# Kernel tuning notes

Hardware: AMD Instinct MI355X
Metric: run time of the kernel (lower is better)

## Reference

```python
import jax, jax.numpy as jnp
import numpy as np

NUM_HEADS = 12

def setup_inputs() -> dict:
    key = jax.random.key(0)
    k1, k2, k3, k4 = jax.random.split(key, 4)
    B, N, C = 64, 197, 768
    x = jax.random.normal(k1, (B, N, C), dtype=jnp.float32)
    w_qkv = jax.random.normal(k2, (3 * C, C), dtype=jnp.float32) * (C ** -0.5)
    w_proj = jax.random.normal(k3, (C, C), dtype=jnp.float32) * (C ** -0.5)
    b_proj = jax.random.normal(k4, (C,), dtype=jnp.float32) * 0.01
    return {"x": x, "w_qkv": w_qkv, "w_proj": w_proj, "b_proj": b_proj}

def reference(x, w_qkv, w_proj, b_proj):
    B, N, C = x.shape
    H = NUM_HEADS
    hd = C // H
    scale = hd ** -0.5
    # qkv linear (no bias): [B,N,3C] -> [3,B,H,N,hd]
    qkv = jnp.einsum('bnc,dc->bnd', x, w_qkv).reshape(B, N, 3, H, hd)
    qkv = jnp.transpose(qkv, (2, 0, 3, 1, 4))
    q, k, v = qkv[0], qkv[1], qkv[2]
    # full attention matrix [B,H,N,N] (materialized, matching the original)
    attn = jax.nn.softmax(jnp.einsum('bhnd,bhmd->bhnm', q, k) * scale, axis=-1)
    # CLS-token attention stats: mean over heads of attn row 0 (patch tokens) -> [B, N-1]
    global_attn = jnp.mean(attn[:, :, 0, 1:], axis=1)
    out = jnp.einsum('bhnm,bhmd->bhnd', attn, v)          # [B,H,N,hd]
    out = jnp.transpose(out, (0, 2, 1, 3)).reshape(B, N, C)
    out = jnp.einsum('bnc,dc->bnd', out, w_proj) + b_proj
    return out, global_attn
```

## Files before the change

kernel.cpp:

```cpp
#include <hip/hip_runtime.h>
#include <math.h>

#define B_   64
#define N_   197
#define C_   768
#define H_   12
#define HD_  64
#define BH_  (B_ * H_)
#define M_   (B_ * N_)

typedef _Float16 half8 __attribute__((ext_vector_type(8)));
typedef float    f32x4 __attribute__((ext_vector_type(4)));

#define XH_OFF   0u
#define WQH_OFF  19365888u
#define WPH_OFF  22904832u
#define QH_OFF   24084480u
#define KH_OFF   43450368u
#define VH_OFF   62816256u
#define OH_OFF   82182144u
#define P0_OFF   101548032u
#define WS_BYTES 102150144u

__device__ __forceinline__ half8 h8zero() {
    half8 z;
    #pragma unroll
    for (int i = 0; i < 8; ++i) z[i] = (_Float16)0;
    return z;
}

__device__ __forceinline__ void async16(const _Float16* g, _Float16* l) {
    __builtin_amdgcn_global_load_lds(
        (const __attribute__((address_space(1))) void*)g,
        (__attribute__((address_space(3))) void*)l,
        16, 0, 0);
}

__device__ __forceinline__ int xcd_swz(int i, int nwg) {
    const int q = nwg >> 3, r = nwg & 7;
    const int xcd = i & 7, j = i >> 3;
    return (xcd < r ? xcd * (q + 1) : r * (q + 1) + (xcd - r) * q) + j;
}

__global__ void k_ws_too_small(float* out, float ws_bytes) { out[0] = -ws_bytes; }

__global__ __launch_bounds__(256) void k_cvt_all(const float* __restrict__ x,
                                                 const float* __restrict__ wq,
                                                 const float* __restrict__ wp,
                                                 _Float16* __restrict__ Xh,
                                                 _Float16* __restrict__ Wqh,
                                                 _Float16* __restrict__ Wph) {
    int i = blockIdx.x * blockDim.x + threadIdx.x;
    const float* src;
    _Float16*    dst;
    if (i < 1210368)      { src = x;  dst = Xh; }
    else if (i < 1431552) { src = wq; dst = Wqh; i -= 1210368; }
    else                  { src = wp; dst = Wph; i -= 1431552; }
    float4 f0 = *(const float4*)(src + (size_t)i * 8);
    float4 f1 = *(const float4*)(src + (size_t)i * 8 + 4);
    half8 h;
    h[0]=(_Float16)f0.x; h[1]=(_Float16)f0.y; h[2]=(_Float16)f0.z; h[3]=(_Float16)f0.w;
    h[4]=(_Float16)f1.x; h[5]=(_Float16)f1.y; h[6]=(_Float16)f1.z; h[7]=(_Float16)f1.w;
    *(half8*)(dst + (size_t)i * 8) = h;
}

__device__ __forceinline__ void mfma_nt_core_256(const _Float16* __restrict__ A,
                                                 const _Float16* __restrict__ B,
                                                 int M, int K, int m0, int n0,
                                                 _Float16* As, _Float16* Bs,
                                                 f32x4 (&acc)[8][4]) {
    const int tid  = threadIdx.x;
    const int lane = tid & 63;
    const int w    = tid >> 6;
    const int wm   = w >> 2, wn = w & 3;
    const int ln   = lane & 15, kq = lane >> 4;

    const int srow = tid >> 3;
    const int kcs  = (((tid & 7) ^ (srow & 7)) << 3);
    int ra00 = m0 +       srow; if (ra00 >= M) ra00 = 0;
    int ra01 = m0 +  64 + srow; if (ra01 >= M) ra01 = 0;
    int ra10 = m0 + 128 + srow; if (ra10 >= M) ra10 = 0;
    int ra11 = m0 + 192 + srow; if (ra11 >= M) ra11 = 0;
    const _Float16* A00 = A + (size_t)ra00 * K + kcs;
    const _Float16* A01 = A + (size_t)ra01 * K + kcs;
    const _Float16* A10 = A + (size_t)ra10 * K + kcs;
    const _Float16* A11 = A + (size_t)ra11 * K + kcs;
    const _Float16* B00 = B + (size_t)(n0 +       srow) * K + kcs;
    const _Float16* B01 = B + (size_t)(n0 +  64 + srow) * K + kcs;
    const _Float16* B10 = B + (size_t)(n0 + 128 + srow) * K + kcs;
    const _Float16* B11 = B + (size_t)(n0 + 192 + srow) * K + kcs;
    const int dOff = w << 9;

    const int kx    = (ln & 7) << 3;
    const int aBase = wm * 8192 + ln * 64;
    const int bBase = (wn >> 1) * 8192 + (wn & 1) * 4096 + ln * 64;

    half8 af[4][2], bf[4][2];

    async16(A00, As + dOff);          async16(A01, As + 4096 + dOff);
    async16(A10, As + 8192 + dOff);   async16(A11, As + 12288 + dOff);
    async16(B00, Bs + dOff);          async16(B01, Bs + 4096 + dOff);
    async16(B10, Bs + 8192 + dOff);   async16(B11, Bs + 12288 + dOff);

    const int NT = K >> 6;
    #pragma unroll 1
    for (int t = 0; t < NT; ++t) {
        const int cur  = (t & 1) << 14;
        const int nb   = 16384 - cur;
        const int koff = (t + 1) << 6;
        const bool pre = (t + 1 < NT);
        const _Float16* Ac = As + cur;
        const _Float16* Bc = Bs + cur;

        if (pre) {
            async16(A00 + koff, As + nb + dOff);
            async16(A01 + koff, As + nb + 4096 + dOff);
            async16(A10 + koff, As + nb + 8192 + dOff);
            async16(A11 + koff, As + nb + 12288 + dOff);
            asm volatile("s_waitcnt vmcnt(4)" ::: "memory");
        } else {
            asm volatile("s_waitcnt vmcnt(0)" ::: "memory");
        }
        __builtin_amdgcn_s_barrier();
        __builtin_amdgcn_sched_barrier(0);
        #pragma unroll
        for (int m4 = 0; m4 < 4; ++m4)
            #pragma unroll
            for (int kk = 0; kk < 2; ++kk)
                af[m4][kk] = *(const half8*)&Ac[aBase + m4 * 1024 + ((kk * 32 + kq * 8) ^ kx)];
        #pragma unroll
        for (int n2 = 0; n2 < 2; ++n2)
            #pragma unroll
            for (int kk = 0; kk < 2; ++kk)
                bf[n2][kk] = *(const half8*)&Bc[bBase + n2 * 1024 + ((kk * 32 + kq * 8) ^ kx)];
        __builtin_amdgcn_s_setprio(1);
        #pragma unroll
        for (int m4 = 0; m4 < 4; ++m4)
            #pragma unroll
            for (int n2 = 0; n2 < 2; ++n2)
                #pragma unroll
                for (int kk = 0; kk < 2; ++kk)
                    acc[m4][n2] = __builtin_amdgcn_mfma_f32_16x16x32_f16(af[m4][kk], bf[n2][kk], acc[m4][n2], 0, 0, 0);
        __builtin_amdgcn_s_setprio(0);
        __builtin_amdgcn_sched_barrier(0);
        __builtin_amdgcn_s_barrier();

        if (pre) {
            async16(B00 + koff, Bs + nb + dOff);
            async16(B01 + koff, Bs + nb + 4096 + dOff);
        }
        #pragma unroll
        for (int n2 = 0; n2 < 2; ++n2)
            #pragma unroll
            for (int kk = 0; kk < 2; ++kk)
                bf[2 + n2][kk] = *(const half8*)&Bc[bBase + (2 + n2) * 1024 + ((kk * 32 + kq * 8) ^ kx)];
        __builtin_amdgcn_s_setprio(1);
        #pragma unroll
        for (int m4 = 0; m4 < 4; ++m4)
            #pragma unroll
            for (int n2 = 0; n2 < 2; ++n2)
                #pragma unroll
                for (int kk = 0; kk < 2; ++kk)
                    acc[m4][2 + n2] = __builtin_amdgcn_mfma_f32_16x16x32_f16(af[m4][kk], bf[2 + n2][kk], acc[m4][2 + n2], 0, 0, 0);
        __builtin_amdgcn_s_setprio(0);
        __builtin_amdgcn_sched_barrier(0);
        __builtin_amdgcn_s_barrier();

        if (pre) {
            async16(B10 + koff, Bs + nb + 8192 + dOff);
            async16(B11 + koff, Bs + nb + 12288 + dOff);
        }
        #pragma unroll
        for (int m4 = 0; m4 < 4; ++m4)
            #pragma unroll
            for (int kk = 0; kk < 2; ++kk)
                af[m4][kk] = *(const half8*)&Ac[aBase + (4 + m4) * 1024 + ((kk * 32 + kq * 8) ^ kx)];
        __builtin_amdgcn_s_setprio(1);
        #pragma unroll
        for (int m4 = 0; m4 < 4; ++m4)
            #pragma unroll
            for (int n2 = 0; n2 < 2; ++n2)
                #pragma unroll
                for (int kk = 0; kk < 2; ++kk)
                    acc[4 + m4][n2] = __builtin_amdgcn_mfma_f32_16x16x32_f16(af[m4][kk], bf[n2][kk], acc[4 + m4][n2], 0, 0, 0);
        __builtin_amdgcn_s_setprio(0);
        __builtin_amdgcn_sched_barrier(0);
        __builtin_amdgcn_s_barrier();

        __builtin_amdgcn_s_setprio(1);
        #pragma unroll
        for (int m4 = 0; m4 < 4; ++m4)
            #pragma unroll
            for (int n2 = 0; n2 < 2; ++n2)
                #pragma unroll
                for (int kk = 0; kk < 2; ++kk)
                    acc[4 + m4][2 + n2] = __builtin_amdgcn_mfma_f32_16x16x32_f16(af[m4][kk], bf[2 + n2][kk], acc[4 + m4][2 + n2], 0, 0, 0);
        __builtin_amdgcn_s_setprio(0);
        asm volatile("s_waitcnt lgkmcnt(0)" ::: "memory");
        __builtin_amdgcn_sched_barrier(0);
        __builtin_amdgcn_s_barrier();
    }
}

__global__ __launch_bounds__(512, 2) void k_qkv_mfma(const _Float16* __restrict__ Xh,
                                                     const _Float16* __restrict__ Wq,
                                                     _Float16* __restrict__ Qh,
                                                     _Float16* __restrict__ Kh,
                                                     _Float16* __restrict__ Vh) {
    __shared__ _Float16 As[32768];
    __shared__ _Float16 Bs[32768];
    const int work = xcd_swz(blockIdx.x, 50 * 9);
    const int m0 = (work / 9) << 8;
    const int n0 = (work % 9) << 8;
    f32x4 acc[8][4] = {};
    mfma_nt_core_256(Xh, Wq, M_, C_, m0, n0, As, Bs, acc);

    const int lane = threadIdx.x & 63;
    const int w    = threadIdx.x >> 6;
    const int wm = w >> 2, wn = w & 3;
    const int ln = lane & 15, kq = lane >> 4;

    _Float16* basep[4];
    float     scl[4];
    #pragma unroll
    for (int ni = 0; ni < 4; ++ni) {
        const int d  = n0 + wn * 64 + ni * 16 + ln;
        const int t3 = d / C_;
        const int rr = d - t3 * C_;
        const int h  = rr >> 6;
        const int e  = rr & 63;
        _Float16* tp = (t3 == 0) ? Qh : (t3 == 1) ? Kh : Vh;
        basep[ni] = tp + (size_t)h * N_ * HD_ + e;
        scl[ni]   = (t3 == 0) ? 0.125f : 1.f;
    }
    #pragma unroll
    for (int mi = 0; mi < 8; ++mi) {
        #pragma unroll
        for (int i = 0; i < 4; ++i) {
            const int m = m0 + wm * 128 + mi * 16 + kq * 4 + i;
            if (m >= M_) continue;
            const int b = m / N_;
            const int n = m - b * N_;
            const size_t rowoff = ((size_t)b * H_ * N_ + n) * HD_;
            #pragma unroll
            for (int ni = 0; ni < 4; ++ni)
                basep[ni][rowoff] = (_Float16)(acc[mi][ni][i] * scl[ni]);
        }
    }
}

__global__ __launch_bounds__(512, 2) void k_proj_mfma(const _Float16* __restrict__ Oh,
                                                      const _Float16* __restrict__ Wp,
                                                      const float* __restrict__ bias,
                                                      float* __restrict__ out) {
    __shared__ _Float16 As[32768];
    __shared__ _Float16 Bs[32768];
    const int work = xcd_swz(blockIdx.x, 50 * 3);
    const int m0 = (work / 3) << 8;
    const int n0 = (work % 3) << 8;
    f32x4 acc[8][4] = {};
    mfma_nt_core_256(Oh, Wp, M_, C_, m0, n0, As, Bs, acc);

    const int lane = threadIdx.x & 63;
    const int w    = threadIdx.x >> 6;
    const int wm = w >> 2, wn = w & 3;
    const int ln = lane & 15, kq = lane >> 4;
    float bv[4];
    #pragma unroll
    for (int ni = 0; ni < 4; ++ni) bv[ni] = bias[n0 + wn * 64 + ni * 16 + ln];
    #pragma unroll
    for (int mi = 0; mi < 8; ++mi) {
        #pragma unroll
        for (int i = 0; i < 4; ++i) {
            const int m = m0 + wm * 128 + mi * 16 + kq * 4 + i;
            if (m >= M_) continue;
            #pragma unroll
            for (int ni = 0; ni < 4; ++ni)
                out[(size_t)m * C_ + n0 + wn * 64 + ni * 16 + ln] = acc[mi][ni][i] + bv[ni];
        }
    }
}

__global__ __launch_bounds__(256) void k_attn(const _Float16* __restrict__ Qh,
                                              const _Float16* __restrict__ Kh,
                                              const _Float16* __restrict__ Vh,
                                              _Float16* __restrict__ Oh,
                                              float* __restrict__ P0) {
    __shared__ _Float16 lds[29824];
    _Float16* Ks = lds;
    _Float16* Pl = lds;
    _Float16* Vt = lds + 14976;

    const int work = xcd_swz(blockIdx.y * 4 + blockIdx.x, 4 * BH_);
    const int bh = work >> 2, rt = work & 3;
    const int b = bh / H_, h = bh - b * H_;
    const int tid = threadIdx.x, wave = tid >> 6, lane = tid & 63;
    const int ln = lane & 15, kq = lane >> 4;
    const size_t kvb = (size_t)bh * N_ * HD_;

    for (int idx = tid; idx < 208 * 8; idx += 256) {
        const int key = idx >> 3, c = (idx & 7) << 3;
        half8 v = (key < N_) ? *(const half8*)(Kh + kvb + (size_t)key * HD_ + c) : h8zero();
        *(half8*)&Ks[key * 72 + c] = v;
    }
    for (int idx = tid; idx < 197 * 8; idx += 256) {
        const int key = idx >> 3, c = (idx & 7) << 3;
        half8 v = *(const half8*)(Vh + kvb + (size_t)key * HD_ + c);
        #pragma unroll
        for (int j = 0; j < 8; ++j) Vt[(c + j) * 232 + key] = v[j];
    }
    for (int idx = tid; idx < 64 * 27; idx += 256) {
        const int d = idx / 27, k = 197 + (idx - d * 27);
        Vt[d * 232 + k] = (_Float16)0;
    }
    const int qrow = rt * 64 + wave * 16 + ln;
    const _Float16* Qp = Qh + kvb + (size_t)((qrow < N_) ? qrow : 0) * HD_ + kq * 8;
    half8 qf0 = *(const half8*)Qp;
    half8 qf1 = *(const half8*)(Qp + 32);
    __syncthreads();

    f32x4 acc[13] = {};
    __builtin_amdgcn_s_setprio(1);
    #pragma unroll
    for (int c = 0; c < 13; ++c) {
        const _Float16* kp = &Ks[(c * 16 + ln) * 72 + kq * 8];
        half8 kf0 = *(const half8*)kp;
        half8 kf1 = *(const half8*)(kp + 32);
        acc[c] = __builtin_amdgcn_mfma_f32_16x16x32_f16(qf0, kf0, acc[c], 0, 0, 0);
        acc[c] = __builtin_amdgcn_mfma_f32_16x16x32_f16(qf1, kf1, acc[c], 0, 0, 0);
    }
    __builtin_amdgcn_s_setprio(0);
    float inv4[4];
    #pragma unroll
    for (int r = 0; r < 4; ++r) {
        float m = -1e30f;
        #pragma unroll
        for (int c = 0; c < 13; ++c) {
            float x = ((c * 16 + ln) < N_) ? acc[c][r] : -1e30f;
            acc[c][r] = x;
            m = fmaxf(m, x);
        }
        m = fmaxf(m, __shfl_xor(m, 1)); m = fmaxf(m, __shfl_xor(m, 2));
        m = fmaxf(m, __shfl_xor(m, 4)); m = fmaxf(m, __shfl_xor(m, 8));
        float s = 0.f;
        #pragma unroll
        for (int c = 0; c < 13; ++c) { float e = __expf(acc[c][r] - m); acc[c][r] = e; s += e; }
        s += __shfl_xor(s, 1); s += __shfl_xor(s, 2);
        s += __shfl_xor(s, 4); s += __shfl_xor(s, 8);
        inv4[r] = 1.f / s;
    }
    __syncthreads();

    _Float16* Pw = Pl + wave * 16 * 232;
    #pragma unroll
    for (int c = 0; c < 13; ++c) {
        const int col = c * 16 + ln;
        #pragma unroll
        for (int r = 0; r < 4; ++r)
            Pw[(kq * 4 + r) * 232 + col] = (_Float16)(acc[c][r] * inv4[r]);
    }
    #pragma unroll
    for (int r = 0; r < 4; ++r) Pw[(kq * 4 + r) * 232 + 208 + ln] = (_Float16)0;

    if (rt == 0 && wave == 0 && kq == 0) {
        #pragma unroll
        for (int c = 0; c < 13; ++c) {
            const int col = c * 16 + ln;
            if (col >= 1 && col < N_) P0[(size_t)bh * 196 + col - 1] = acc[c][0] * inv4[0];
        }
    }
    __syncthreads();

    f32x4 o4[4] = {};
    __builtin_amdgcn_s_setprio(1);
    for (int t = 0; t < 7; ++t) {
        half8 pf = *(const half8*)&Pw[ln * 232 + kq * 8 + 32 * t];
        #pragma unroll
        for (int n = 0; n < 4; ++n) {
            half8 vf = *(const half8*)&Vt[(n * 16 + ln) * 232 + kq * 8 + 32 * t];
            o4[n] = __builtin_amdgcn_mfma_f32_16x16x32_f16(pf, vf, o4[n], 0, 0, 0);
        }
    }
    __builtin_amdgcn_s_setprio(0);
    const int g0 = rt * 64 + wave * 16 + kq * 4;
    #pragma unroll
    for (int r = 0; r < 4; ++r) {
        const int g = g0 + r;
        if (g >= N_) continue;
        _Float16* op = Oh + ((size_t)b * N_ + g) * C_ + h * HD_;
        #pragma unroll
        for (int n = 0; n < 4; ++n) op[n * 16 + ln] = (_Float16)o4[n][r];
    }
}

__global__ void k_gattn(const float* __restrict__ P0, float* __restrict__ out2) {
    const int idx = blockIdx.x * blockDim.x + threadIdx.x;
    const int b = idx / (N_ - 1), m = idx - b * (N_ - 1);
    float s = 0.f;
    #pragma unroll
    for (int h = 0; h < H_; ++h) s += P0[((size_t)(b * H_ + h)) * 196 + m];
    out2[idx] = s * (1.f / H_);
}

extern "C" void kernel_launch(void* const* d_in, const int* in_sizes, int n_in,
                              void* d_out, int out_size, void* d_ws, size_t ws_size,
                              hipStream_t stream) {
    const float* x      = (const float*)d_in[0];
    const float* w_qkv  = (const float*)d_in[1];
    const float* w_proj = (const float*)d_in[2];
    const float* b_proj = (const float*)d_in[3];
    float* out = (float*)d_out;
    char* ws   = (char*)d_ws;

    if (ws_size < (size_t)WS_BYTES) {
        k_ws_too_small<<<1, 1, 0, stream>>>(out, (float)ws_size);
        return;
    }

    _Float16* Xh  = (_Float16*)(ws + XH_OFF);
    _Float16* Wqh = (_Float16*)(ws + WQH_OFF);
    _Float16* Wph = (_Float16*)(ws + WPH_OFF);
    _Float16* Qh  = (_Float16*)(ws + QH_OFF);
    _Float16* Kh  = (_Float16*)(ws + KH_OFF);
    _Float16* Vh  = (_Float16*)(ws + VH_OFF);
    _Float16* Oh  = (_Float16*)(ws + OH_OFF);
    float*    P0  = (float*)   (ws + P0_OFF);

    k_cvt_all<<<5880, 256, 0, stream>>>(x, w_qkv, w_proj, Xh, Wqh, Wph);

    k_qkv_mfma <<<dim3(450), 512, 0, stream>>>(Xh, Wqh, Qh, Kh, Vh);
    k_attn     <<<dim3(4, BH_), 256, 0, stream>>>(Qh, Kh, Vh, Oh, P0);
    k_gattn    <<<dim3(49),     256, 0, stream>>>(P0, out + (size_t)M_ * C_);
    k_proj_mfma<<<dim3(150), 512, 0, stream>>>(Oh, Wph, b_proj, out);
}
```

Before: 249.7 us.

## Load K/V once per head in attention and retile projection GEMM to 128x128

```diff
diff --git a/kernel.cpp b/kernel.cpp
--- a/kernel.cpp
+++ b/kernel.cpp
@@ -202,6 +202,60 @@
     }
 }
 
+__device__ __forceinline__ void mfma_nt_core_h(const _Float16* __restrict__ A,
+                                               const _Float16* __restrict__ B,
+                                               int M, int K, int m0, int n0,
+                                               _Float16* As, _Float16* Bs,
+                                               f32x4 (&acc)[4][4]) {
+    const int tid  = threadIdx.x;
+    const int wave = tid >> 6, lane = tid & 63;
+    const int wr   = (wave >> 1) << 6;
+    const int wc   = (wave & 1) << 6;
+    const int ln   = lane & 15, kq = lane >> 4;
+
+    const int row0 = tid >> 2;
+    const int ch0  = (tid & 3) << 3;
+    int ar0 = m0 + row0;        if (ar0 >= M) ar0 = 0;
+    int ar1 = m0 + 64 + row0;   if (ar1 >= M) ar1 = 0;
+    const _Float16* A0 = A + (size_t)ar0 * K + ch0;
+    const _Float16* A1 = A + (size_t)ar1 * K + ch0;
+    const _Float16* B0 = B + (size_t)(n0 + row0) * K + ch0;
+    const _Float16* B1 = B + (size_t)(n0 + 64 + row0) * K + ch0;
+    _Float16* AsD = As + (wave << 9);
+    _Float16* BsD = Bs + (wave << 9);
+
+    async16(A0, AsD);        async16(A1, AsD + 2048);
+    async16(B0, BsD);        async16(B1, BsD + 2048);
+    __syncthreads();
+
+    int cur = 0;
+    for (int k0 = 0; k0 < K; k0 += 32) {
+        const int nxt = cur ^ 1;
+        if (k0 + 32 < K) {
+            const int nb = nxt << 12;
+            async16(A0 + k0 + 32, AsD + nb);
+            async16(A1 + k0 + 32, AsD + nb + 2048);
+            async16(B0 + k0 + 32, BsD + nb);
+            async16(B1 + k0 + 32, BsD + nb + 2048);
+        }
+        const _Float16* Ac = As + (cur << 12);
+        const _Float16* Bc = Bs + (cur << 12);
+        half8 af[4], bf[4];
+        #pragma unroll
+        for (int t = 0; t < 4; ++t) {
+            af[t] = *(const half8*)&Ac[(wr + t * 16 + ln) * 32 + kq * 8];
+            bf[t] = *(const half8*)&Bc[(wc + t * 16 + ln) * 32 + kq * 8];
+        }
+        #pragma unroll
+        for (int i = 0; i < 4; ++i)
+            #pragma unroll
+            for (int j = 0; j < 4; ++j)
+                acc[i][j] = __builtin_amdgcn_mfma_f32_16x16x32_f16(af[i], bf[j], acc[i][j], 0, 0, 0);
+        __syncthreads();
+        cur = nxt;
+    }
+}
+
 __global__ __launch_bounds__(512, 2) void k_qkv_mfma(const _Float16* __restrict__ Xh,
                                                      const _Float16* __restrict__ Wq,
                                                      _Float16* __restrict__ Qh,
@@ -249,34 +303,34 @@
     }
 }
 
-__global__ __launch_bounds__(512, 2) void k_proj_mfma(const _Float16* __restrict__ Oh,
-                                                      const _Float16* __restrict__ Wp,
-                                                      const float* __restrict__ bias,
-                                                      float* __restrict__ out) {
-    __shared__ _Float16 As[32768];
-    __shared__ _Float16 Bs[32768];
-    const int work = xcd_swz(blockIdx.x, 50 * 3);
-    const int m0 = (work / 3) << 8;
-    const int n0 = (work % 3) << 8;
-    f32x4 acc[8][4] = {};
-    mfma_nt_core_256(Oh, Wp, M_, C_, m0, n0, As, Bs, acc);
+__global__ __launch_bounds__(256) void k_proj_mfma(const _Float16* __restrict__ Oh,
+                                                   const _Float16* __restrict__ Wp,
+                                                   const float* __restrict__ bias,
+                                                   float* __restrict__ out) {
+    __shared__ _Float16 As[2 * 4096];
+    __shared__ _Float16 Bs[2 * 4096];
+    const int work = xcd_swz(blockIdx.y * 6 + blockIdx.x, 6 * 99);
+    const int m0 = (work / 6) << 7;
+    const int n0 = (work % 6) << 7;
+    f32x4 acc[4][4] = {};
+    mfma_nt_core_h(Oh, Wp, M_, C_, m0, n0, As, Bs, acc);
 
     const int lane = threadIdx.x & 63;
-    const int w    = threadIdx.x >> 6;
-    const int wm = w >> 2, wn = w & 3;
+    const int wave = threadIdx.x >> 6;
+    const int wr = (wave >> 1) << 6, wc = (wave & 1) << 6;
     const int ln = lane & 15, kq = lane >> 4;
     float bv[4];
     #pragma unroll
-    for (int ni = 0; ni < 4; ++ni) bv[ni] = bias[n0 + wn * 64 + ni * 16 + ln];
+    for (int nt = 0; nt < 4; ++nt) bv[nt] = bias[n0 + wc + nt * 16 + ln];
     #pragma unroll
-    for (int mi = 0; mi < 8; ++mi) {
+    for (int mt = 0; mt < 4; ++mt) {
         #pragma unroll
         for (int i = 0; i < 4; ++i) {
-            const int m = m0 + wm * 128 + mi * 16 + kq * 4 + i;
+            const int m = m0 + wr + mt * 16 + kq * 4 + i;
             if (m >= M_) continue;
             #pragma unroll
-            for (int ni = 0; ni < 4; ++ni)
-                out[(size_t)m * C_ + n0 + wn * 64 + ni * 16 + ln] = acc[mi][ni][i] + bv[ni];
+            for (int nt = 0; nt < 4; ++nt)
+                out[(size_t)m * C_ + n0 + wc + nt * 16 + ln] = acc[mt][nt][i] + bv[nt];
         }
     }
 }
@@ -286,110 +340,127 @@
                                               const _Float16* __restrict__ Vh,
                                               _Float16* __restrict__ Oh,
                                               float* __restrict__ P0) {
-    __shared__ _Float16 lds[29824];
+    __shared__ _Float16 lds[39936];
     _Float16* Ks = lds;
-    _Float16* Pl = lds;
-    _Float16* Vt = lds + 14976;
-
-    const int work = xcd_swz(blockIdx.y * 4 + blockIdx.x, 4 * BH_);
-    const int bh = work >> 2, rt = work & 3;
+    _Float16* Vt = lds + 13312;
+    _Float16* Pl = lds + 26624;
+
+    const int bh = blockIdx.x;
     const int b = bh / H_, h = bh - b * H_;
     const int tid = threadIdx.x, wave = tid >> 6, lane = tid & 63;
     const int ln = lane & 15, kq = lane >> 4;
     const size_t kvb = (size_t)bh * N_ * HD_;
 
     for (int idx = tid; idx < 208 * 8; idx += 256) {
-        const int key = idx >> 3, c = (idx & 7) << 3;
-        half8 v = (key < N_) ? *(const half8*)(Kh + kvb + (size_t)key * HD_ + c) : h8zero();
-        *(half8*)&Ks[key * 72 + c] = v;
+        const int key = idx >> 3, c8 = idx & 7;
+        half8 v = (key < N_) ? *(const half8*)(Kh + kvb + (size_t)key * HD_ + c8 * 8) : h8zero();
+        *(half8*)&Ks[key * 64 + ((c8 ^ (key & 7)) << 3)] = v;
     }
     for (int idx = tid; idx < 197 * 8; idx += 256) {
         const int key = idx >> 3, c = (idx & 7) << 3;
         half8 v = *(const half8*)(Vh + kvb + (size_t)key * HD_ + c);
         #pragma unroll
-        for (int j = 0; j < 8; ++j) Vt[(c + j) * 232 + key] = v[j];
-    }
-    for (int idx = tid; idx < 64 * 27; idx += 256) {
-        const int d = idx / 27, k = 197 + (idx - d * 27);
-        Vt[d * 232 + k] = (_Float16)0;
-    }
-    const int qrow = rt * 64 + wave * 16 + ln;
-    const _Float16* Qp = Qh + kvb + (size_t)((qrow < N_) ? qrow : 0) * HD_ + kq * 8;
-    half8 qf0 = *(const half8*)Qp;
-    half8 qf1 = *(const half8*)(Qp + 32);
+        for (int j = 0; j < 8; ++j) Vt[(c + j) * 208 + key] = v[j];
+    }
+    for (int idx = tid; idx < 64 * 11; idx += 256) {
+        const int d = idx / 11, k = 197 + (idx - d * 11);
+        Vt[d * 208 + k] = (_Float16)0;
+    }
     __syncthreads();
 
-    f32x4 acc[13] = {};
-    __builtin_amdgcn_s_setprio(1);
-    #pragma unroll
-    for (int c = 0; c < 13; ++c) {
-        const _Float16* kp = &Ks[(c * 16 + ln) * 72 + kq * 8];
-        half8 kf0 = *(const half8*)kp;
-        half8 kf1 = *(const half8*)(kp + 32);
-        acc[c] = __builtin_amdgcn_mfma_f32_16x16x32_f16(qf0, kf0, acc[c], 0, 0, 0);
-        acc[c] = __builtin_amdgcn_mfma_f32_16x16x32_f16(qf1, kf1, acc[c], 0, 0, 0);
-    }
-    __builtin_amdgcn_s_setprio(0);
-    float inv4[4];
-    #pragma unroll
-    for (int r = 0; r < 4; ++r) {
-        float m = -1e30f;
+    _Float16* Pw = Pl + wave * 16 * 208;
+    const int swz = ln & 7;
+
+    for (int rt = 0; rt < 4; ++rt) {
+        if (rt * 64 + wave * 16 >= N_) continue;
+
+        const int qrow = rt * 64 + wave * 16 + ln;
+        const _Float16* Qp = Qh + kvb + (size_t)((qrow < N_) ? qrow : 0) * HD_ + kq * 8;
+        half8 qf0 = *(const half8*)Qp;
+        half8 qf1 = *(const half8*)(Qp + 32);
+
+        f32x4 acc[13] = {};
+        __builtin_amdgcn_s_setprio(1);
         #pragma unroll
         for (int c = 0; c < 13; ++c) {
-            float x = ((c * 16 + ln) < N_) ? acc[c][r] : -1e30f;
-            acc[c][r] = x;
-            m = fmaxf(m, x);
-        }
-        m = fmaxf(m, __shfl_xor(m, 1)); m = fmaxf(m, __shfl_xor(m, 2));
-        m = fmaxf(m, __shfl_xor(m, 4)); m = fmaxf(m, __shfl_xor(m, 8));
-        float s = 0.f;
-        #pragma unroll
-        for (int c = 0; c < 13; ++c) { float e = __expf(acc[c][r] - m); acc[c][r] = e; s += e; }
-        s += __shfl_xor(s, 1); s += __shfl_xor(s, 2);
-        s += __shfl_xor(s, 4); s += __shfl_xor(s, 8);
-        inv4[r] = 1.f / s;
-    }
-    __syncthreads();
-
-    _Float16* Pw = Pl + wave * 16 * 232;
-    #pragma unroll
-    for (int c = 0; c < 13; ++c) {
-        const int col = c * 16 + ln;
-        #pragma unroll
-        for (int r = 0; r < 4; ++r)
-            Pw[(kq * 4 + r) * 232 + col] = (_Float16)(acc[c][r] * inv4[r]);
-    }
-    #pragma unroll
-    for (int r = 0; r < 4; ++r) Pw[(kq * 4 + r) * 232 + 208 + ln] = (_Float16)0;
-
-    if (rt == 0 && wave == 0 && kq == 0) {
+            const _Float16* kp = &Ks[(c * 16 + ln) * 64];
+            half8 kf0 = *(const half8*)(kp + ((kq ^ swz) << 3));
+            half8 kf1 = *(const half8*)(kp + (((4 + kq) ^ swz) << 3));
+            acc[c] = __builtin_amdgcn_mfma_f32_16x16x32_f16(qf0, kf0, acc[c], 0, 0, 0);
+            acc[c] = __builtin_amdgcn_mfma_f32_16x16x32_f16(qf1, kf1, acc[c], 0, 0, 0);
+        }
+        __builtin_amdgcn_s_setprio(0);
+
+        float inv4[4];
+        #pragma unroll
+        for (int r = 0; r < 4; ++r) {
+            float m = -1e30f;
+            #pragma unroll
+            for (int c = 0; c < 13; ++c) {
+                float x = ((c * 16 + ln) < N_) ? acc[c][r] : -1e30f;
+                acc[c][r] = x;
+                m = fmaxf(m, x);
+            }
+            m = fmaxf(m, __shfl_xor(m, 1)); m = fmaxf(m, __shfl_xor(m, 2));
+            m = fmaxf(m, __shfl_xor(m, 4)); m = fmaxf(m, __shfl_xor(m, 8));
+            float s = 0.f;
+            #pragma unroll
+            for (int c = 0; c < 13; ++c) { float e = __expf(acc[c][r] - m); acc[c][r] = e; s += e; }
+            s += __shfl_xor(s, 1); s += __shfl_xor(s, 2);
+            s += __shfl_xor(s, 4); s += __shfl_xor(s, 8);
+            inv4[r] = 1.f / s;
+        }
+
         #pragma unroll
         for (int c = 0; c < 13; ++c) {
             const int col = c * 16 + ln;
-            if (col >= 1 && col < N_) P0[(size_t)bh * 196 + col - 1] = acc[c][0] * inv4[0];
-        }
-    }
-    __syncthreads();
-
-    f32x4 o4[4] = {};
-    __builtin_amdgcn_s_setprio(1);
-    for (int t = 0; t < 7; ++t) {
-        half8 pf = *(const half8*)&Pw[ln * 232 + kq * 8 + 32 * t];
-        #pragma unroll
-        for (int n = 0; n < 4; ++n) {
-            half8 vf = *(const half8*)&Vt[(n * 16 + ln) * 232 + kq * 8 + 32 * t];
-            o4[n] = __builtin_amdgcn_mfma_f32_16x16x32_f16(pf, vf, o4[n], 0, 0, 0);
-        }
-    }
-    __builtin_amdgcn_s_setprio(0);
-    const int g0 = rt * 64 + wave * 16 + kq * 4;
-    #pragma unroll
-    for (int r = 0; r < 4; ++r) {
-        const int g = g0 + r;
-        if (g >= N_) continue;
-        _Float16* op = Oh + ((size_t)b * N_ + g) * C_ + h * HD_;
-        #pragma unroll
-        for (int n = 0; n < 4; ++n) op[n * 16 + ln] = (_Float16)o4[n][r];
+            #pragma unroll
+            for (int r = 0; r < 4; ++r)
+                Pw[(kq * 4 + r) * 208 + col] = (_Float16)(acc[c][r] * inv4[r]);
+        }
+
+        if (rt == 0 && wave == 0 && kq == 0) {
+            #pragma unroll
+            for (int c = 0; c < 13; ++c) {
+                const int col = c * 16 + ln;
+                if (col >= 1 && col < N_) P0[(size_t)bh * 196 + col - 1] = acc[c][0] * inv4[0];
+            }
+        }
+        asm volatile("s_waitcnt lgkmcnt(0)" ::: "memory");
+        __builtin_amdgcn_sched_barrier(0);
+
+        f32x4 o4[4] = {};
+        __builtin_amdgcn_s_setprio(1);
+        #pragma unroll
+        for (int t = 0; t < 6; ++t) {
+            half8 pf = *(const half8*)&Pw[ln * 208 + kq * 8 + 32 * t];
+            #pragma unroll
+            for (int n = 0; n < 4; ++n) {
+                half8 vf = *(const half8*)&Vt[(n * 16 + ln) * 208 + kq * 8 + 32 * t];
+                o4[n] = __builtin_amdgcn_mfma_f32_16x16x32_f16(pf, vf, o4[n], 0, 0, 0);
+            }
+        }
+        {
+            const int off6 = (kq < 2) ? (192 + kq * 8) : 0;
+            half8 pf = *(const half8*)&Pw[ln * 208 + off6];
+            if (kq >= 2) pf = h8zero();
+            #pragma unroll
+            for (int n = 0; n < 4; ++n) {
+                half8 vf = *(const half8*)&Vt[(n * 16 + ln) * 208 + off6];
+                o4[n] = __builtin_amdgcn_mfma_f32_16x16x32_f16(pf, vf, o4[n], 0, 0, 0);
+            }
+        }
+        __builtin_amdgcn_s_setprio(0);
+
+        const int g0 = rt * 64 + wave * 16 + kq * 4;
+        #pragma unroll
+        for (int r = 0; r < 4; ++r) {
+            const int g = g0 + r;
+            if (g >= N_) continue;
+            _Float16* op = Oh + ((size_t)b * N_ + g) * C_ + h * HD_;
+            #pragma unroll
+            for (int n = 0; n < 4; ++n) op[n * 16 + ln] = (_Float16)o4[n][r];
+        }
     }
 }
 
@@ -428,8 +499,8 @@
 
     k_cvt_all<<<5880, 256, 0, stream>>>(x, w_qkv, w_proj, Xh, Wqh, Wph);
 
-    k_qkv_mfma <<<dim3(450), 512, 0, stream>>>(Xh, Wqh, Qh, Kh, Vh);
-    k_attn     <<<dim3(4, BH_), 256, 0, stream>>>(Qh, Kh, Vh, Oh, P0);
-    k_gattn    <<<dim3(49),     256, 0, stream>>>(P0, out + (size_t)M_ * C_);
-    k_proj_mfma<<<dim3(150), 512, 0, stream>>>(Oh, Wph, b_proj, out);
-}
+    k_qkv_mfma <<<dim3(450),   512, 0, stream>>>(Xh, Wqh, Qh, Kh, Vh);
+    k_attn     <<<dim3(BH_),   256, 0, stream>>>(Qh, Kh, Vh, Oh, P0);
+    k_gattn    <<<dim3(49),    256, 0, stream>>>(P0, out + (size_t)M_ * C_);
+    k_proj_mfma<<<dim3(6, 99), 256, 0, stream>>>(Oh, Wph, b_proj, out);
+}
```

Measured after the change: 226.3 us. 1.1x faster.
